# Kernel tuning notes

Hardware: AMD Instinct MI355X
Metric: run time of the kernel (lower is better)

The kernel has to match this reference:

```python
import jax, jax.numpy as jnp
import numpy as np

TEMPERATURE = 0.2

def setup_inputs() -> dict:
    key = jax.random.key(0)
    k1, k2 = jax.random.split(key)
    B, D = 4096, 128
    emb_i = jax.random.normal(k1, (B, D), dtype=jnp.float32)
    emb_j = jax.random.normal(k2, (B, D), dtype=jnp.float32)
    return {"emb_i": emb_i, "emb_j": emb_j}

def reference(emb_i, emb_j):
    # L2-normalize each embedding row, concat -> z: [2B, D]
    z_i = emb_i / jnp.linalg.norm(emb_i, axis=1, keepdims=True)
    z_j = emb_j / jnp.linalg.norm(emb_j, axis=1, keepdims=True)
    z = jnp.concatenate([z_i, z_j], axis=0)          # [2B, D]
    N2 = z.shape[0]
    N = N2 // 2
    # cosine similarity of normalized vectors == dot product
    sim = z @ z.T                                    # [2B, 2B]
    logits = sim / TEMPERATURE
    # denominator excludes only the diagonal (k != i)
    diag_mask = jnp.eye(N2, dtype=bool)
    masked = jnp.where(diag_mask, -jnp.inf, logits)
    lse = jax.nn.logsumexp(masked, axis=1)           # [2B]
    # positive pair for row i is i+N (mod 2N)
    pos_idx = jnp.concatenate([jnp.arange(N) + N, jnp.arange(N)])
    pos_logits = jnp.take_along_axis(logits, pos_idx[:, None], axis=1)[:, 0]
    # loss = (1/2N) * sum_i -log( exp(pos_i) / sum_{k!=i} exp(logits[i,k]) )
    loss = jnp.mean(lse - pos_logits)
    return loss
```

## Files before the change

### kernel.cpp

```cpp
#include <hip/hip_runtime.h>
#include <hip/hip_bf16.h>

typedef __attribute__((ext_vector_type(8))) short bf16x8;
typedef __attribute__((ext_vector_type(4))) float f32x4;

#define EXP_SCALE 7.213475204444817f

__device__ __forceinline__ float fast_exp2(float x) {
#if __has_builtin(__builtin_amdgcn_exp2f)
  return __builtin_amdgcn_exp2f(x);
#else
  return exp2f(x);
#endif
}

__device__ __forceinline__ unsigned short f32_to_bf16(float f) {
  unsigned int u = __float_as_uint(f);
  unsigned int r = (u + 0x7FFFu + ((u >> 16) & 1u)) >> 16;
  return (unsigned short)r;
}


__global__ __launch_bounds__(256) void k_normalize(
    const float* __restrict__ emb_i, const float* __restrict__ emb_j,
    unsigned short* __restrict__ z, float* __restrict__ out)
{
  if (blockIdx.x == 0 && threadIdx.x == 0) out[0] = 0.0f;
  const int w = threadIdx.x >> 6;
  const int lane = threadIdx.x & 63;
  const int row = (blockIdx.x << 2) + w;
  const float* src = (row < 4096) ? (emb_i + row * 128) : (emb_j + (row - 4096) * 128);
  float2 v = reinterpret_cast<const float2*>(src)[lane];
  float ss = v.x * v.x + v.y * v.y;
  #pragma unroll
  for (int m = 1; m < 64; m <<= 1) ss += __shfl_xor(ss, m, 64);
  float rinv = 1.0f / sqrtf(ss);
  ushort2 st;
  st.x = f32_to_bf16(v.x * rinv);
  st.y = f32_to_bf16(v.y * rinv);
  const int e = lane << 1;
  const int kk = e >> 5;
  const int q = (e >> 3) & 3;
  const int rem = e & 7;
  const int tile = row >> 4;
  const int c = row & 15;
  unsigned short* dst = z + tile * 2048 + kk * 512 + ((q << 4) + c) * 8 + rem;
  *reinterpret_cast<ushort2*>(dst) = st;
}

__global__ __launch_bounds__(256, 3) void k_simlse(
    const unsigned short* __restrict__ z,
    float* __restrict__ rpart,
    float* __restrict__ cpart,
    float* __restrict__ rowpos)
{
  const int w = threadIdx.x >> 6;
  const int lane = threadIdx.x & 63;
  const int q = lane >> 4;
  const int c = lane & 15;

  int ch = 0;
  while ((int)blockIdx.x >= 4 * (ch + 1) * (ch + 2)) ++ch;
  const int rb = blockIdx.x - 4 * ch * (ch + 1);
  const int R0 = rb << 6;
  const bool upper = (rb < (ch << 3));

  __shared__ short smem[8192];
  {
    const unsigned short* zA = z + (R0 >> 4) * 2048;
    #pragma unroll
    for (int j = 0; j < 4; ++j) {
      const int v = (j << 8) + threadIdx.x;
      *reinterpret_cast<bf16x8*>(&smem[v << 3]) =
          *reinterpret_cast<const bf16x8*>(zA + (v << 3));
    }
  }
  __syncthreads();
  bf16x8 a[4][4];
  #pragma unroll
  for (int rg = 0; rg < 4; ++rg)
    #pragma unroll
    for (int kk = 0; kk < 4; ++kk)
      a[rg][kk] = *reinterpret_cast<const bf16x8*>(
          &smem[rg * 2048 + kk * 512 + (lane << 3)]);

  float acc[4][4];
  #pragma unroll
  for (int rg = 0; rg < 4; ++rg)
    #pragma unroll
    for (int e = 0; e < 4; ++e) acc[rg][e] = 0.0f;
  float pacc[4] = {0.f, 0.f, 0.f, 0.f};

  __shared__ float lsum[4][64];
  __shared__ float lpos[4][16];

  const int ct0 = (ch << 5) + w;
  const unsigned short* bwave = z + ct0 * 2048 + (lane << 3);

  const int pos0t = ((R0 + 4096) & 8191) >> 4;
  const int ipb = ((pos0t >> 5) == ch) ? ((pos0t & 31) >> 2) : -99;

  bf16x8 b0[4], b1[4];
  auto ldb = [&](bf16x8 (&dst)[4], int idx) {
    const unsigned short* p = bwave + idx * 8192;
    dst[0] = *reinterpret_cast<const bf16x8*>(p);
    dst[1] = *reinterpret_cast<const bf16x8*>(p + 512);
    dst[2] = *reinterpret_cast<const bf16x8*>(p + 1024);
    dst[3] = *reinterpret_cast<const bf16x8*>(p + 1536);
  };

  auto process = [&](const bf16x8 (&bb)[4], int i) {
    f32x4 cc[4];
    #pragma unroll
    for (int rr = 0; rr < 4; ++rr) cc[rr] = f32x4{0.f, 0.f, 0.f, 0.f};
    #pragma unroll
    for (int kk = 0; kk < 4; ++kk)
      #pragma unroll
      for (int rr = 0; rr < 4; ++rr)
        cc[rr] = __builtin_amdgcn_mfma_f32_16x16x32_bf16(
            a[rr][kk], bb[kk], cc[rr], 0, 0, 0);
    float colp0 = 0.0f, colp1 = 0.0f;
    #pragma unroll
    for (int rr = 0; rr < 4; ++rr)
      #pragma unroll
      for (int e = 0; e < 4; ++e) {
        float t = fast_exp2(__builtin_fmaf(cc[rr][e], EXP_SCALE, -EXP_SCALE));
        acc[rr][e] += t;
        if (upper) { if (rr & 1) colp1 += t; else colp0 += t; }
      }
    if (upper) {
      float colp = colp0 + colp1;
      colp += __shfl_xor(colp, 16, 64);
      colp += __shfl_xor(colp, 32, 64);
      if (lane < 16)
        cpart[(rb << 13) + (((ct0 + (i << 2)) << 4) + c)] = colp;
    }
    if (i == ipb) {
      #pragma unroll
      for (int rr = 0; rr < 4; ++rr) {
        if (rr == w) {
          #pragma unroll
          for (int e = 0; e < 4; ++e)
            if (c == ((q << 2) + e)) pacc[e] = cc[rr][e] * 5.0f;
        }
      }
    }
  };

  ldb(b0, 0);
  #pragma unroll 1
  for (int i = 0; i < 8; i += 2) {
    ldb(b1, i + 1);
    process(b0, i);
    if (i + 2 < 8) ldb(b0, i + 2);
    process(b1, i + 1);
  }

  #pragma unroll
  for (int m = 1; m < 16; m <<= 1) {
    #pragma unroll
    for (int rg = 0; rg < 4; ++rg)
      #pragma unroll
      for (int e = 0; e < 4; ++e)
        acc[rg][e] += __shfl_xor(acc[rg][e], m, 64);
    #pragma unroll
    for (int e = 0; e < 4; ++e) pacc[e] += __shfl_xor(pacc[e], m, 64);
  }

  if (c == 0) {
    #pragma unroll
    for (int rg = 0; rg < 4; ++rg)
      #pragma unroll
      for (int e = 0; e < 4; ++e)
        lsum[w][rg * 16 + (q << 2) + e] = acc[rg][e];
    #pragma unroll
    for (int e = 0; e < 4; ++e) lpos[w][(q << 2) + e] = pacc[e];
  }
  __syncthreads();

  if (threadIdx.x < 64) {
    const int t = threadIdx.x;
    float s = lsum[0][t] + lsum[1][t] + lsum[2][t] + lsum[3][t];
    rpart[(ch << 13) + R0 + t] = s;
    if (ipb != -99)
      rowpos[R0 + t] = lpos[t >> 4][t & 15];
  }
}

__global__ __launch_bounds__(256) void k_finish(
    const float* __restrict__ rpart, const float* __restrict__ cpart,
    const float* __restrict__ rowpos, float* __restrict__ out)
{
  const int r = blockIdx.x * 256 + threadIdx.x;
  const int chr = r >> 9;
  float t0 = -1.0f, t1 = 0.0f;
  for (int ch = chr; ch < 16; ++ch) t0 += rpart[(ch << 13) + r];
  const int nrb = chr << 3;
  #pragma unroll 4
  for (int rb = 0; rb < nrb; rb += 2) {
    t0 += cpart[(rb << 13) + r];
    t1 += cpart[((rb + 1) << 13) + r];
  }
  float tot = t0 + t1;
  float v = 5.0f + logf(tot) - rowpos[r & 4095];
  #pragma unroll
  for (int m = 1; m < 64; m <<= 1) v += __shfl_xor(v, m, 64);
  __shared__ float red[4];
  if ((threadIdx.x & 63) == 0) red[threadIdx.x >> 6] = v;
  __syncthreads();
  if (threadIdx.x == 0)
    atomicAdd(out, (red[0] + red[1] + red[2] + red[3]) * (1.0f / 8192.0f));
}

extern "C" void kernel_launch(void* const* d_in, const int* in_sizes, int n_in,
                              void* d_out, int out_size, void* d_ws, size_t ws_size,
                              hipStream_t stream) {
  const float* emb_i = (const float*)d_in[0];
  const float* emb_j = (const float*)d_in[1];
  unsigned short* z = (unsigned short*)d_ws;
  float* rpart = (float*)((char*)d_ws + (2 << 20));
  float* cpart = rpart + 16 * 8192;
  float* rowpos = cpart + 128 * 8192;
  float* out = (float*)d_out;

  k_normalize<<<2048, 256, 0, stream>>>(emb_i, emb_j, z, out);
  k_simlse<<<1088, 256, 0, stream>>>(z, rpart, cpart, rowpos);
  k_finish<<<32, 256, 0, stream>>>(rpart, cpart, rowpos, out);
}
```

Measured before the change: 83.11 us.

## Vectorize normalize stores, load A fragments directly, defer column-sum reductions

```diff
diff --git a/kernel.cpp b/kernel.cpp
--- a/kernel.cpp
+++ b/kernel.cpp
@@ -26,26 +26,26 @@
     unsigned short* __restrict__ z, float* __restrict__ out)
 {
   if (blockIdx.x == 0 && threadIdx.x == 0) out[0] = 0.0f;
-  const int w = threadIdx.x >> 6;
-  const int lane = threadIdx.x & 63;
-  const int row = (blockIdx.x << 2) + w;
+  const int t = threadIdx.x;
+  const int c = t >> 4;
+  const int sub = t & 15;
+  const int row = (blockIdx.x << 4) + c;
   const float* src = (row < 4096) ? (emb_i + row * 128) : (emb_j + (row - 4096) * 128);
-  float2 v = reinterpret_cast<const float2*>(src)[lane];
-  float ss = v.x * v.x + v.y * v.y;
-  #pragma unroll
-  for (int m = 1; m < 64; m <<= 1) ss += __shfl_xor(ss, m, 64);
+  float4 v0 = reinterpret_cast<const float4*>(src)[sub * 2];
+  float4 v1 = reinterpret_cast<const float4*>(src)[sub * 2 + 1];
+  float ss = v0.x*v0.x + v0.y*v0.y + v0.z*v0.z + v0.w*v0.w
+           + v1.x*v1.x + v1.y*v1.y + v1.z*v1.z + v1.w*v1.w;
+  #pragma unroll
+  for (int m = 1; m < 16; m <<= 1) ss += __shfl_xor(ss, m, 64);
   float rinv = 1.0f / sqrtf(ss);
-  ushort2 st;
-  st.x = f32_to_bf16(v.x * rinv);
-  st.y = f32_to_bf16(v.y * rinv);
-  const int e = lane << 1;
-  const int kk = e >> 5;
-  const int q = (e >> 3) & 3;
-  const int rem = e & 7;
-  const int tile = row >> 4;
-  const int c = row & 15;
-  unsigned short* dst = z + tile * 2048 + kk * 512 + ((q << 4) + c) * 8 + rem;
-  *reinterpret_cast<ushort2*>(dst) = st;
+  unsigned short st[8];
+  st[0] = f32_to_bf16(v0.x * rinv); st[1] = f32_to_bf16(v0.y * rinv);
+  st[2] = f32_to_bf16(v0.z * rinv); st[3] = f32_to_bf16(v0.w * rinv);
+  st[4] = f32_to_bf16(v1.x * rinv); st[5] = f32_to_bf16(v1.y * rinv);
+  st[6] = f32_to_bf16(v1.z * rinv); st[7] = f32_to_bf16(v1.w * rinv);
+  unsigned short* dst = z + blockIdx.x * 2048 + (sub >> 2) * 512 +
+                        (((sub & 3) << 4) + c) * 8;
+  *reinterpret_cast<bf16x8*>(dst) = *reinterpret_cast<bf16x8*>(st);
 }
 
 __global__ __launch_bounds__(256, 3) void k_simlse(
@@ -65,24 +65,15 @@
   const int R0 = rb << 6;
   const bool upper = (rb < (ch << 3));
 
-  __shared__ short smem[8192];
+  bf16x8 a[4][4];
   {
-    const unsigned short* zA = z + (R0 >> 4) * 2048;
-    #pragma unroll
-    for (int j = 0; j < 4; ++j) {
-      const int v = (j << 8) + threadIdx.x;
-      *reinterpret_cast<bf16x8*>(&smem[v << 3]) =
-          *reinterpret_cast<const bf16x8*>(zA + (v << 3));
-    }
-  }
-  __syncthreads();
-  bf16x8 a[4][4];
-  #pragma unroll
-  for (int rg = 0; rg < 4; ++rg)
-    #pragma unroll
-    for (int kk = 0; kk < 4; ++kk)
-      a[rg][kk] = *reinterpret_cast<const bf16x8*>(
-          &smem[rg * 2048 + kk * 512 + (lane << 3)]);
+    const unsigned short* ap = z + (R0 >> 4) * 2048 + (lane << 3);
+    #pragma unroll
+    for (int rg = 0; rg < 4; ++rg)
+      #pragma unroll
+      for (int kk = 0; kk < 4; ++kk)
+        a[rg][kk] = *reinterpret_cast<const bf16x8*>(ap + rg * 2048 + kk * 512);
+  }
 
   float acc[4][4];
   #pragma unroll
@@ -90,6 +81,9 @@
     #pragma unroll
     for (int e = 0; e < 4; ++e) acc[rg][e] = 0.0f;
   float pacc[4] = {0.f, 0.f, 0.f, 0.f};
+  float colp[8];
+  #pragma unroll
+  for (int i = 0; i < 8; ++i) colp[i] = 0.0f;
 
   __shared__ float lsum[4][64];
   __shared__ float lpos[4][16];
@@ -119,22 +113,16 @@
       for (int rr = 0; rr < 4; ++rr)
         cc[rr] = __builtin_amdgcn_mfma_f32_16x16x32_bf16(
             a[rr][kk], bb[kk], cc[rr], 0, 0, 0);
-    float colp0 = 0.0f, colp1 = 0.0f;
+    float cp0 = 0.0f, cp1 = 0.0f;
     #pragma unroll
     for (int rr = 0; rr < 4; ++rr)
       #pragma unroll
       for (int e = 0; e < 4; ++e) {
-        float t = fast_exp2(__builtin_fmaf(cc[rr][e], EXP_SCALE, -EXP_SCALE));
-        acc[rr][e] += t;
-        if (upper) { if (rr & 1) colp1 += t; else colp0 += t; }
+        float tv = fast_exp2(__builtin_fmaf(cc[rr][e], EXP_SCALE, -EXP_SCALE));
+        acc[rr][e] += tv;
+        if (upper) { if (rr & 1) cp1 += tv; else cp0 += tv; }
       }
-    if (upper) {
-      float colp = colp0 + colp1;
-      colp += __shfl_xor(colp, 16, 64);
-      colp += __shfl_xor(colp, 32, 64);
-      if (lane < 16)
-        cpart[(rb << 13) + (((ct0 + (i << 2)) << 4) + c)] = colp;
-    }
+    if (upper) colp[i] = cp0 + cp1;
     if (i == ipb) {
       #pragma unroll
       for (int rr = 0; rr < 4; ++rr) {
@@ -154,6 +142,17 @@
     process(b0, i);
     if (i + 2 < 8) ldb(b0, i + 2);
     process(b1, i + 1);
+  }
+
+  if (upper) {
+    #pragma unroll
+    for (int i = 0; i < 8; ++i) {
+      float v = colp[i];
+      v += __shfl_xor(v, 16, 64);
+      v += __shfl_xor(v, 32, 64);
+      if (lane < 16)
+        cpart[(rb << 13) + (((ct0 + (i << 2)) << 4) + c)] = v;
+    }
   }
 
   #pragma unroll
@@ -223,7 +222,7 @@
   float* rowpos = cpart + 128 * 8192;
   float* out = (float*)d_out;
 
-  k_normalize<<<2048, 256, 0, stream>>>(emb_i, emb_j, z, out);
+  k_normalize<<<512, 256, 0, stream>>>(emb_i, emb_j, z, out);
   k_simlse<<<1088, 256, 0, stream>>>(z, rpart, cpart, rowpos);
   k_finish<<<32, 256, 0, stream>>>(rpart, cpart, rowpos, out);
 }
```

New measurement: 82.91 us. About the same (-0.2%).
